# Performance work log

Measured on AMD Instinct MI355X. Metric: run time of the kernel, lower is better.

## Reference

```python
import jax, jax.numpy as jnp
import numpy as np

N_WIRES = 8
N_QLAYERS = 1
DIM = 1 << N_WIRES  # 256

# bits[s, w] = w-th bit of basis state s; wire 0 is the MOST significant bit
# (torchquantum stores states as [bsz, 2, 2, ..., 2] with wire i at axis i+1)
_BITS = ((np.arange(DIM)[:, None] >> (N_WIRES - 1 - np.arange(N_WIRES))) & 1).astype(np.float32)


def setup_inputs() -> dict:
    key = jax.random.key(0)
    ks = jax.random.split(key, 5)
    pi = float(np.pi)
    return {
        "input_features": jax.random.normal(ks[0], (4, 4096, N_WIRES), jnp.float32),
        "params_ry1": jax.random.uniform(ks[1], (N_QLAYERS, N_WIRES), jnp.float32, -pi, pi),
        "params_crz1": jax.random.uniform(ks[2], (N_QLAYERS, N_WIRES), jnp.float32, -pi, pi),
        "params_ry2": jax.random.uniform(ks[3], (N_QLAYERS, N_WIRES), jnp.float32, -pi, pi),
        "params_crz2": jax.random.uniform(ks[4], (N_QLAYERS, N_WIRES), jnp.float32, -pi, pi),
    }


def _apply_ry(state, wire, theta):
    """Apply RY(theta) = [[c,-s],[s,c]] (c=cos(theta/2)) on `wire`.
    theta: scalar (shared param) or [B] (batched encoder angle)."""
    B = state.shape[0]
    c = jnp.cos(theta * 0.5)
    s = jnp.sin(theta * 0.5)
    if jnp.ndim(theta):  # per-batch angle
        c = c[:, None, None]
        s = s[:, None, None]
    st = state.reshape(B, 1 << wire, 2, -1)
    a, b = st[:, :, 0, :], st[:, :, 1, :]
    return jnp.stack([c * a - s * b, s * a + c * b], axis=2).reshape(B, DIM)


def _crz_block_diag(controls, targets, thetas, bits):
    """Fused diagonal of a commuting block of CRZ gates.
    CRZ(c,t,th) = diag over basis: 1 if bit_c==0 else exp(+/- i th/2) for bit_t=1/0.
    exponent contribution: bit_c * th * (bit_t - 0.5)."""
    expo = (bits[:, controls] * (bits[:, targets] - 0.5)) @ thetas  # [DIM]
    return jnp.exp(1j * expo).astype(jnp.complex64)


def _vqc_forward(x, params_ry1, params_crz1, params_ry2, params_crz2):
    B = x.shape[0]
    bits = jnp.asarray(_BITS)
    # |0...0>
    state = jnp.zeros((B, DIM), jnp.complex64).at[:, 0].set(1.0)

    idx = np.arange(N_WIRES)
    ctrl1, tgt1 = idx, (idx + 1) % N_WIRES  # crz block 1: wires [i, i+1]
    ctrl2, tgt2 = idx, (idx - 1) % N_WIRES  # crz block 2: wires [i, i-1]

    for k in range(N_QLAYERS):
        # tensor-product encoder: RY(x_i) on wire i
        for i in range(N_WIRES):
            state = _apply_ry(state, i, x[:, i])
        # CRZ ring (all diagonal -> fused)
        state = state * _crz_block_diag(ctrl1, tgt1, params_crz1[k], bits)[None, :]
        # trainable RY layer 1
        for i in range(N_WIRES):
            state = _apply_ry(state, i, params_ry1[k, i])
        # reverse CRZ ring (diagonal -> fused)
        state = state * _crz_block_diag(ctrl2, tgt2, params_crz2[k], bits)[None, :]
        # trainable RY layer 2
        for i in range(N_WIRES):
            state = _apply_ry(state, i, params_ry2[k, i])

    # PauliZ expectation on every wire: <Z_w> = sum_s |amp_s|^2 * (1 - 2*bit_w(s))
    probs = (state.real ** 2 + state.imag ** 2)  # [B, DIM]
    signs = 1.0 - 2.0 * bits                      # [DIM, N_WIRES]
    return probs @ signs                          # [B, N_WIRES]


def reference(input_features, params_ry1, params_crz1, params_ry2, params_crz2):
    bsz, slen, fz = input_features.shape
    x = input_features.reshape(-1, fz)
    out = _vqc_forward(x, params_ry1, params_crz1, params_ry2, params_crz2)
    return out.reshape(bsz, slen, fz)
```

## Files before the change

kernel.cpp:

```cpp
#include <hip/hip_runtime.h>
#include <math.h>

#define NW 8

typedef float v2f __attribute__((ext_vector_type(2)));

__device__ __forceinline__ v2f mk2(float a, float b) { v2f r; r.x = a; r.y = b; return r; }

template<int CTRL>
__device__ __forceinline__ float dpp_x(float v) {
    return __int_as_float(
        __builtin_amdgcn_update_dpp(0, __float_as_int(v), CTRL, 0xF, 0xF, true));
}
template<int CTRL>
__device__ __forceinline__ v2f dpp2(v2f v) {
    v2f r;
    r.x = dpp_x<CTRL>(v.x);
    r.y = dpp_x<CTRL>(v.y);
    return r;
}
#define XCH1(v) dpp2<0xB1>(v)
#define XCH2(v) dpp2<0x4E>(v)
#define XCH8(v) dpp2<0x128>(v)

__global__ __launch_bounds__(256, 2) void vqc_kernel(
    const float* __restrict__ x,
    const float* __restrict__ ry1,
    const float* __restrict__ crz1,
    const float* __restrict__ ry2,
    const float* __restrict__ crz2,
    float* __restrict__ out,
    int B)
{
    __shared__ __align__(16) float Tc1[288], Ts1[288], Tc2[288], Ts2[288];

    const int t = threadIdx.x;
    {
        const int n = t;
        float e1 = 0.f, e2 = 0.f;
#pragma unroll
        for (int i = 0; i < NW; ++i) {
            float bc  = (float)((n >> (7 - i)) & 1);
            float bt1 = (float)((n >> (7 - ((i + 1) & 7))) & 1);
            float bt2 = (float)((n >> (7 - ((i + 7) & 7))) & 1);
            e1 += bc * crz1[i] * (bt1 - 0.5f);
            e2 += bc * crz2[i] * (bt2 - 0.5f);
        }
        const int j = n & 31;
        const int u = (((n >> 7) & 1) << 2) | (((n >> 6) & 1) << 1) | ((n >> 5) & 1);
        const int idx = u * 36 + j;
        float s, c;
        __sincosf(e1, &s, &c);  Tc1[idx] = c;  Ts1[idx] = s;
        __sincosf(e2, &s, &c);  Tc2[idx] = c;  Ts2[idx] = s;
    }
    __syncthreads();

    const int lane = t & 63;
    const int u = ((lane & 1) << 2) | (((lane >> 1) & 1) << 1) | ((lane >> 3) & 1);
    const int g = ((lane >> 3) & 6) | ((lane >> 2) & 1);

    float rc1[8], rs1[8], rc2[8], rs2[8];
#pragma unroll
    for (int i = 0; i < 8; ++i) {
        __sincosf(0.5f * ry1[i], &rs1[i], &rc1[i]);
        __sincosf(0.5f * ry2[i], &rs2[i], &rc2[i]);
    }

    const float* pc1 = &Tc1[u * 36];
    const float* ps1 = &Ts1[u * 36];
    const float* pc2 = &Tc2[u * 36];
    const float* ps2 = &Ts2[u * 36];

    const int wavesPerBlock = blockDim.x >> 6;
    const int gwave = blockIdx.x * wavesPerBlock + (t >> 6);
    const int b  = gwave * 8 + g;
    const int bl = (b < B) ? b : (B - 1);

    const float4* xp = (const float4*)(x + (size_t)bl * NW);
    float4 xa = xp[0], xb = xp[1];
    float cs[8], sn[8];
    __sincosf(0.5f * xa.x, &sn[0], &cs[0]);
    __sincosf(0.5f * xa.y, &sn[1], &cs[1]);
    __sincosf(0.5f * xa.z, &sn[2], &cs[2]);
    __sincosf(0.5f * xa.w, &sn[3], &cs[3]);
    __sincosf(0.5f * xb.x, &sn[4], &cs[4]);
    __sincosf(0.5f * xb.y, &sn[5], &cs[5]);
    __sincosf(0.5f * xb.z, &sn[6], &cs[6]);
    __sincosf(0.5f * xb.w, &sn[7], &cs[7]);

    float pcf = ((lane & 1) ? sn[0] : cs[0])
              * ((lane & 2) ? sn[1] : cs[1])
              * ((lane & 8) ? sn[2] : cs[2]);

    float t2[2], t4[4], t8[8], t16[16];
    t2[0] = pcf * cs[3];  t2[1] = pcf * sn[3];
#pragma unroll
    for (int k = 0; k < 2; ++k)  { t4[2*k]  = t2[k] * cs[4];  t4[2*k+1]  = t2[k] * sn[4]; }
#pragma unroll
    for (int k = 0; k < 4; ++k)  { t8[2*k]  = t4[k] * cs[5];  t8[2*k+1]  = t4[k] * sn[5]; }
#pragma unroll
    for (int k = 0; k < 8; ++k)  { t16[2*k] = t8[k] * cs[6];  t16[2*k+1] = t8[k] * sn[6]; }

    const v2f cw7 = mk2(cs[7], sn[7]);
    v2f aP[16];
#pragma unroll
    for (int k = 0; k < 16; ++k) aP[k] = mk2(t16[k], t16[k]) * cw7;

    v2f reP[16], imP[16];
#pragma unroll
    for (int q = 0; q < 8; ++q) {
        float4 cq = *(const float4*)&pc1[4 * q];
        float4 sq = *(const float4*)&ps1[4 * q];
        v2f cl = mk2(cq.x, cq.y), ch = mk2(cq.z, cq.w);
        v2f sl = mk2(sq.x, sq.y), sh = mk2(sq.z, sq.w);
        reP[2*q]   = aP[2*q]   * cl;  imP[2*q]   = aP[2*q]   * sl;
        reP[2*q+1] = aP[2*q+1] * ch;  imP[2*q+1] = aP[2*q+1] * sh;
    }

#define CROSS_WIRE(RC, RS, WI, LBIT, EXCH)                                  \
    { float c_ = RC[WI], s_ = RS[WI];                                       \
      float se_ = (lane & LBIT) ? s_ : -s_;                                 \
      v2f cv = mk2(c_, c_), sev = mk2(se_, se_);                            \
      _Pragma("unroll")                                                     \
      for (int k = 0; k < 16; ++k) {                                        \
          v2f pre = EXCH(reP[k]);                                           \
          v2f pim = EXCH(imP[k]);                                           \
          reP[k] = reP[k] * cv + pre * sev;                                 \
          imP[k] = imP[k] * cv + pim * sev;                                 \
      } }

#define INLANE_WIRE(RC, RS, WI, M)                                          \
    { float c_ = RC[WI], s_ = RS[WI];                                       \
      v2f cv = mk2(c_, c_), sv = mk2(s_, s_);                               \
      _Pragma("unroll")                                                     \
      for (int k = 0; k < 16; ++k) if (!(k & M)) {                          \
          int h = k | M;                                                    \
          v2f rl = reP[k], rh = reP[h], il = imP[k], ih = imP[h];           \
          reP[k] = rl * cv - rh * sv;  reP[h] = rl * sv + rh * cv;          \
          imP[k] = il * cv - ih * sv;  imP[h] = il * sv + ih * cv;          \
      } }

#define WIRE7(RC, RS)                                                       \
    { float c_ = RC[7], s_ = RS[7];                                         \
      v2f cv = mk2(c_, c_), sev = mk2(-s_, s_);                             \
      _Pragma("unroll")                                                     \
      for (int k = 0; k < 16; ++k) {                                        \
          v2f r = reP[k], i = imP[k];                                       \
          v2f rsw = mk2(r.y, r.x), isw = mk2(i.y, i.x);                     \
          reP[k] = r * cv + rsw * sev;                                      \
          imP[k] = i * cv + isw * sev;                                      \
      } }

#define RY_LAYER(RC, RS)                                                    \
    do {                                                                    \
        CROSS_WIRE(RC, RS, 0, 1, XCH1);                                     \
        CROSS_WIRE(RC, RS, 1, 2, XCH2);                                     \
        CROSS_WIRE(RC, RS, 2, 8, XCH8);                                     \
        INLANE_WIRE(RC, RS, 3, 8);                                          \
        INLANE_WIRE(RC, RS, 4, 4);                                          \
        INLANE_WIRE(RC, RS, 5, 2);                                          \
        INLANE_WIRE(RC, RS, 6, 1);                                          \
        WIRE7(RC, RS);                                                      \
    } while (0)

    RY_LAYER(rc1, rs1);

#pragma unroll
    for (int q = 0; q < 8; ++q) {
        float4 cq = *(const float4*)&pc2[4 * q];
        float4 sq = *(const float4*)&ps2[4 * q];
        v2f cl = mk2(cq.x, cq.y), ch = mk2(cq.z, cq.w);
        v2f sl = mk2(sq.x, sq.y), sh = mk2(sq.z, sq.w);
        v2f r, i;
        r = reP[2*q];   i = imP[2*q];
        reP[2*q]   = r * cl - i * sl;  imP[2*q]   = r * sl + i * cl;
        r = reP[2*q+1]; i = imP[2*q+1];
        reP[2*q+1] = r * ch - i * sh;  imP[2*q+1] = r * sh + i * ch;
    }

    RY_LAYER(rc2, rs2);

    v2f pP[16];
#pragma unroll
    for (int k = 0; k < 16; ++k) pP[k] = reP[k] * reP[k] + imP[k] * imP[k];

    v2f s1v[8], dv6 = mk2(0.f, 0.f);
#pragma unroll
    for (int k = 0; k < 8; ++k) { s1v[k] = pP[2*k] + pP[2*k+1]; dv6 += pP[2*k] - pP[2*k+1]; }
    v2f s2v[4], dv5 = mk2(0.f, 0.f);
#pragma unroll
    for (int k = 0; k < 4; ++k) { s2v[k] = s1v[2*k] + s1v[2*k+1]; dv5 += s1v[2*k] - s1v[2*k+1]; }
    v2f s3v[2], dv4 = mk2(0.f, 0.f);
#pragma unroll
    for (int k = 0; k < 2; ++k) { s3v[k] = s2v[2*k] + s2v[2*k+1]; dv4 += s2v[2*k] - s2v[2*k+1]; }
    v2f sv0 = s3v[0] + s3v[1];
    v2f dv3 = s3v[0] - s3v[1];

    float v0 = sv0.x + sv0.y, d7 = sv0.x - sv0.y;
    float d3 = dv3.x + dv3.y, d4 = dv4.x + dv4.y;
    float d5 = dv5.x + dv5.y, d6 = dv6.x + dv6.y;

    v2f w1 = mk2(v0, d3), w2 = mk2(d4, d5), w3 = mk2(d6, d7);
#define BFLY_R(EXCH, M)                                                     \
    { v2f o1 = EXCH(w1), o2 = EXCH(w2), o3 = EXCH(w3);                      \
      if (lane & M) { w1 = o1 - w1; w2 = o2 - w2; w3 = o3 - w3; }           \
      else          { w1 = o1 + w1; w2 = o2 + w2; w3 = o3 + w3; } }
    BFLY_R(XCH1, 1);
    BFLY_R(XCH2, 2);
    BFLY_R(XCH8, 8);
#undef BFLY_R

    if (b < B) {
        const int loc = lane & 11;
        float* ob = out + (size_t)b * NW;
        if      (loc == 0) { ob[3] = w1.y; *(float4*)(ob + 4) = make_float4(w2.x, w2.y, w3.x, w3.y); }
        else if (loc == 1) ob[0] = w1.x;
        else if (loc == 2) ob[1] = w1.x;
        else if (loc == 8) ob[2] = w1.x;
    }
#undef RY_LAYER
#undef CROSS_WIRE
#undef INLANE_WIRE
#undef WIRE7
}

extern "C" void kernel_launch(void* const* d_in, const int* in_sizes, int n_in,
                              void* d_out, int out_size, void* d_ws, size_t ws_size,
                              hipStream_t stream) {
    const float* x    = (const float*)d_in[0];
    const float* ry1  = (const float*)d_in[1];
    const float* crz1 = (const float*)d_in[2];
    const float* ry2  = (const float*)d_in[3];
    const float* crz2 = (const float*)d_in[4];
    float* out = (float*)d_out;

    int B = in_sizes[0] / NW;
    int blocks = (B + 31) / 32;
    if (blocks < 1) blocks = 1;
    vqc_kernel<<<blocks, 256, 0, stream>>>(x, ry1, crz1, ry2, crz2, out, B);
}
```

Baseline: 67.85 us.

## Spread each statevector over 16 lanes using permlane32 swap to halve registers

Wire 3 moves from being held inside a lane to being spread across lane halves, using a permlane32 swap (or a shuffle fallback). Each wave now simulates 4 samples instead of 8, and each lane holds 8 complex pairs instead of 16. Launch bounds rise to 4 blocks per SM, the grid doubles, and the CRZ tables are re-laid out for 16 lanes. The aim is lower register pressure and higher occupancy, at the cost of extra cross-lane exchanges and twice as many waves doing the same total work.

```diff
diff --git a/kernel.cpp b/kernel.cpp
--- a/kernel.cpp
+++ b/kernel.cpp
@@ -4,6 +4,7 @@
 #define NW 8
 
 typedef float v2f __attribute__((ext_vector_type(2)));
+typedef int   v2i __attribute__((ext_vector_type(2)));
 
 __device__ __forceinline__ v2f mk2(float a, float b) { v2f r; r.x = a; r.y = b; return r; }
 
@@ -23,7 +24,27 @@
 #define XCH2(v) dpp2<0x4E>(v)
 #define XCH8(v) dpp2<0x128>(v)
 
-__global__ __launch_bounds__(256, 2) void vqc_kernel(
+__device__ __forceinline__ float rfl(float v) {
+    return __int_as_float(__builtin_amdgcn_readfirstlane(__float_as_int(v)));
+}
+
+__device__ __forceinline__ float xch32f(float v, int lane) {
+#if __has_builtin(__builtin_amdgcn_permlane32_swap)
+    v2i r = __builtin_amdgcn_permlane32_swap(__float_as_int(v), __float_as_int(v),
+                                             false, false);
+    return __int_as_float((lane & 32) ? r[0] : r[1]);
+#else
+    return __shfl_xor(v, 32, 64);
+#endif
+}
+__device__ __forceinline__ v2f xch32_2(v2f v, int lane) {
+    v2f r;
+    r.x = xch32f(v.x, lane);
+    r.y = xch32f(v.y, lane);
+    return r;
+}
+
+__global__ __launch_bounds__(256, 4) void vqc_kernel(
     const float* __restrict__ x,
     const float* __restrict__ ry1,
     const float* __restrict__ crz1,
@@ -32,7 +53,7 @@
     float* __restrict__ out,
     int B)
 {
-    __shared__ __align__(16) float Tc1[288], Ts1[288], Tc2[288], Ts2[288];
+    __shared__ __align__(16) float Tc1[320], Ts1[320], Tc2[320], Ts2[320];
 
     const int t = threadIdx.x;
     {
@@ -46,9 +67,9 @@
             e1 += bc * crz1[i] * (bt1 - 0.5f);
             e2 += bc * crz2[i] * (bt2 - 0.5f);
         }
-        const int j = n & 31;
-        const int u = (((n >> 7) & 1) << 2) | (((n >> 6) & 1) << 1) | ((n >> 5) & 1);
-        const int idx = u * 36 + j;
+        const int j = n & 15;
+        const int u = n >> 4;
+        const int idx = u * 20 + j;
         float s, c;
         __sincosf(e1, &s, &c);  Tc1[idx] = c;  Ts1[idx] = s;
         __sincosf(e2, &s, &c);  Tc2[idx] = c;  Ts2[idx] = s;
@@ -56,24 +77,26 @@
     __syncthreads();
 
     const int lane = t & 63;
-    const int u = ((lane & 1) << 2) | (((lane >> 1) & 1) << 1) | ((lane >> 3) & 1);
-    const int g = ((lane >> 3) & 6) | ((lane >> 2) & 1);
+    const int u = ((lane & 1) << 3) | (((lane >> 1) & 1) << 2)
+                | (((lane >> 3) & 1) << 1) | ((lane >> 5) & 1);
+    const int g = ((lane >> 3) & 2) | ((lane >> 2) & 1);
 
     float rc1[8], rs1[8], rc2[8], rs2[8];
 #pragma unroll
     for (int i = 0; i < 8; ++i) {
-        __sincosf(0.5f * ry1[i], &rs1[i], &rc1[i]);
-        __sincosf(0.5f * ry2[i], &rs2[i], &rc2[i]);
-    }
-
-    const float* pc1 = &Tc1[u * 36];
-    const float* ps1 = &Ts1[u * 36];
-    const float* pc2 = &Tc2[u * 36];
-    const float* ps2 = &Ts2[u * 36];
+        float s, c;
+        __sincosf(0.5f * ry1[i], &s, &c);  rc1[i] = rfl(c);  rs1[i] = rfl(s);
+        __sincosf(0.5f * ry2[i], &s, &c);  rc2[i] = rfl(c);  rs2[i] = rfl(s);
+    }
+
+    const float* pc1 = &Tc1[u * 20];
+    const float* ps1 = &Ts1[u * 20];
+    const float* pc2 = &Tc2[u * 20];
+    const float* ps2 = &Ts2[u * 20];
 
     const int wavesPerBlock = blockDim.x >> 6;
     const int gwave = blockIdx.x * wavesPerBlock + (t >> 6);
-    const int b  = gwave * 8 + g;
+    const int b  = gwave * 4 + g;
     const int bl = (b < B) ? b : (B - 1);
 
     const float4* xp = (const float4*)(x + (size_t)bl * NW);
@@ -88,27 +111,26 @@
     __sincosf(0.5f * xb.z, &sn[6], &cs[6]);
     __sincosf(0.5f * xb.w, &sn[7], &cs[7]);
 
-    float pcf = ((lane & 1) ? sn[0] : cs[0])
-              * ((lane & 2) ? sn[1] : cs[1])
-              * ((lane & 8) ? sn[2] : cs[2]);
-
-    float t2[2], t4[4], t8[8], t16[16];
-    t2[0] = pcf * cs[3];  t2[1] = pcf * sn[3];
-#pragma unroll
-    for (int k = 0; k < 2; ++k)  { t4[2*k]  = t2[k] * cs[4];  t4[2*k+1]  = t2[k] * sn[4]; }
-#pragma unroll
-    for (int k = 0; k < 4; ++k)  { t8[2*k]  = t4[k] * cs[5];  t8[2*k+1]  = t4[k] * sn[5]; }
-#pragma unroll
-    for (int k = 0; k < 8; ++k)  { t16[2*k] = t8[k] * cs[6];  t16[2*k+1] = t8[k] * sn[6]; }
+    float pcf = ((lane & 1)  ? sn[0] : cs[0])
+              * ((lane & 2)  ? sn[1] : cs[1])
+              * ((lane & 8)  ? sn[2] : cs[2])
+              * ((lane & 32) ? sn[3] : cs[3]);
+
+    float t2[2], t4[4], t8[8];
+    t2[0] = pcf * cs[4];  t2[1] = pcf * sn[4];
+#pragma unroll
+    for (int k = 0; k < 2; ++k) { t4[2*k] = t2[k] * cs[5];  t4[2*k+1] = t2[k] * sn[5]; }
+#pragma unroll
+    for (int k = 0; k < 4; ++k) { t8[2*k] = t4[k] * cs[6];  t8[2*k+1] = t4[k] * sn[6]; }
 
     const v2f cw7 = mk2(cs[7], sn[7]);
-    v2f aP[16];
-#pragma unroll
-    for (int k = 0; k < 16; ++k) aP[k] = mk2(t16[k], t16[k]) * cw7;
-
-    v2f reP[16], imP[16];
-#pragma unroll
-    for (int q = 0; q < 8; ++q) {
+    v2f aP[8];
+#pragma unroll
+    for (int k = 0; k < 8; ++k) aP[k] = mk2(t8[k], t8[k]) * cw7;
+
+    v2f reP[8], imP[8];
+#pragma unroll
+    for (int q = 0; q < 4; ++q) {
         float4 cq = *(const float4*)&pc1[4 * q];
         float4 sq = *(const float4*)&ps1[4 * q];
         v2f cl = mk2(cq.x, cq.y), ch = mk2(cq.z, cq.w);
@@ -122,18 +144,30 @@
       float se_ = (lane & LBIT) ? s_ : -s_;                                 \
       v2f cv = mk2(c_, c_), sev = mk2(se_, se_);                            \
       _Pragma("unroll")                                                     \
-      for (int k = 0; k < 16; ++k) {                                        \
+      for (int k = 0; k < 8; ++k) {                                         \
           v2f pre = EXCH(reP[k]);                                           \
           v2f pim = EXCH(imP[k]);                                           \
           reP[k] = reP[k] * cv + pre * sev;                                 \
           imP[k] = imP[k] * cv + pim * sev;                                 \
       } }
 
+#define CROSS_WIRE32(RC, RS, WI)                                            \
+    { float c_ = RC[WI], s_ = RS[WI];                                       \
+      float se_ = (lane & 32) ? s_ : -s_;                                   \
+      v2f cv = mk2(c_, c_), sev = mk2(se_, se_);                            \
+      _Pragma("unroll")                                                     \
+      for (int k = 0; k < 8; ++k) {                                         \
+          v2f pre = xch32_2(reP[k], lane);                                  \
+          v2f pim = xch32_2(imP[k], lane);                                  \
+          reP[k] = reP[k] * cv + pre * sev;                                 \
+          imP[k] = imP[k] * cv + pim * sev;                                 \
+      } }
+
 #define INLANE_WIRE(RC, RS, WI, M)                                          \
     { float c_ = RC[WI], s_ = RS[WI];                                       \
       v2f cv = mk2(c_, c_), sv = mk2(s_, s_);                               \
       _Pragma("unroll")                                                     \
-      for (int k = 0; k < 16; ++k) if (!(k & M)) {                          \
+      for (int k = 0; k < 8; ++k) if (!(k & M)) {                           \
           int h = k | M;                                                    \
           v2f rl = reP[k], rh = reP[h], il = imP[k], ih = imP[h];           \
           reP[k] = rl * cv - rh * sv;  reP[h] = rl * sv + rh * cv;          \
@@ -144,7 +178,7 @@
     { float c_ = RC[7], s_ = RS[7];                                         \
       v2f cv = mk2(c_, c_), sev = mk2(-s_, s_);                             \
       _Pragma("unroll")                                                     \
-      for (int k = 0; k < 16; ++k) {                                        \
+      for (int k = 0; k < 8; ++k) {                                         \
           v2f r = reP[k], i = imP[k];                                       \
           v2f rsw = mk2(r.y, r.x), isw = mk2(i.y, i.x);                     \
           reP[k] = r * cv + rsw * sev;                                      \
@@ -156,7 +190,7 @@
         CROSS_WIRE(RC, RS, 0, 1, XCH1);                                     \
         CROSS_WIRE(RC, RS, 1, 2, XCH2);                                     \
         CROSS_WIRE(RC, RS, 2, 8, XCH8);                                     \
-        INLANE_WIRE(RC, RS, 3, 8);                                          \
+        CROSS_WIRE32(RC, RS, 3);                                            \
         INLANE_WIRE(RC, RS, 4, 4);                                          \
         INLANE_WIRE(RC, RS, 5, 2);                                          \
         INLANE_WIRE(RC, RS, 6, 1);                                          \
@@ -166,7 +200,7 @@
     RY_LAYER(rc1, rs1);
 
 #pragma unroll
-    for (int q = 0; q < 8; ++q) {
+    for (int q = 0; q < 4; ++q) {
         float4 cq = *(const float4*)&pc2[4 * q];
         float4 sq = *(const float4*)&ps2[4 * q];
         v2f cl = mk2(cq.x, cq.y), ch = mk2(cq.z, cq.w);
@@ -180,27 +214,24 @@
 
     RY_LAYER(rc2, rs2);
 
-    v2f pP[16];
-#pragma unroll
-    for (int k = 0; k < 16; ++k) pP[k] = reP[k] * reP[k] + imP[k] * imP[k];
-
-    v2f s1v[8], dv6 = mk2(0.f, 0.f);
-#pragma unroll
-    for (int k = 0; k < 8; ++k) { s1v[k] = pP[2*k] + pP[2*k+1]; dv6 += pP[2*k] - pP[2*k+1]; }
-    v2f s2v[4], dv5 = mk2(0.f, 0.f);
-#pragma unroll
-    for (int k = 0; k < 4; ++k) { s2v[k] = s1v[2*k] + s1v[2*k+1]; dv5 += s1v[2*k] - s1v[2*k+1]; }
-    v2f s3v[2], dv4 = mk2(0.f, 0.f);
-#pragma unroll
-    for (int k = 0; k < 2; ++k) { s3v[k] = s2v[2*k] + s2v[2*k+1]; dv4 += s2v[2*k] - s2v[2*k+1]; }
-    v2f sv0 = s3v[0] + s3v[1];
-    v2f dv3 = s3v[0] - s3v[1];
+    v2f pP[8];
+#pragma unroll
+    for (int k = 0; k < 8; ++k) pP[k] = reP[k] * reP[k] + imP[k] * imP[k];
+
+    v2f s1v[4], dv6 = mk2(0.f, 0.f);
+#pragma unroll
+    for (int k = 0; k < 4; ++k) { s1v[k] = pP[2*k] + pP[2*k+1]; dv6 += pP[2*k] - pP[2*k+1]; }
+    v2f s2v[2], dv5 = mk2(0.f, 0.f);
+#pragma unroll
+    for (int k = 0; k < 2; ++k) { s2v[k] = s1v[2*k] + s1v[2*k+1]; dv5 += s1v[2*k] - s1v[2*k+1]; }
+    v2f sv0 = s2v[0] + s2v[1];
+    v2f dv4 = s2v[0] - s2v[1];
 
     float v0 = sv0.x + sv0.y, d7 = sv0.x - sv0.y;
-    float d3 = dv3.x + dv3.y, d4 = dv4.x + dv4.y;
+    float d4 = dv4.x + dv4.y;
     float d5 = dv5.x + dv5.y, d6 = dv6.x + dv6.y;
 
-    v2f w1 = mk2(v0, d3), w2 = mk2(d4, d5), w3 = mk2(d6, d7);
+    v2f w1 = mk2(v0, d4), w2 = mk2(d5, d6), w3 = mk2(d7, 0.f);
 #define BFLY_R(EXCH, M)                                                     \
     { v2f o1 = EXCH(w1), o2 = EXCH(w2), o3 = EXCH(w3);                      \
       if (lane & M) { w1 = o1 - w1; w2 = o2 - w2; w3 = o3 - w3; }           \
@@ -208,18 +239,23 @@
     BFLY_R(XCH1, 1);
     BFLY_R(XCH2, 2);
     BFLY_R(XCH8, 8);
+    { v2f o1 = xch32_2(w1, lane), o2 = xch32_2(w2, lane), o3 = xch32_2(w3, lane);
+      if (lane & 32) { w1 = o1 - w1; w2 = o2 - w2; w3 = o3 - w3; }
+      else           { w1 = o1 + w1; w2 = o2 + w2; w3 = o3 + w3; } }
 #undef BFLY_R
 
     if (b < B) {
-        const int loc = lane & 11;
+        const int loc = lane & 43;
         float* ob = out + (size_t)b * NW;
-        if      (loc == 0) { ob[3] = w1.y; *(float4*)(ob + 4) = make_float4(w2.x, w2.y, w3.x, w3.y); }
-        else if (loc == 1) ob[0] = w1.x;
-        else if (loc == 2) ob[1] = w1.x;
-        else if (loc == 8) ob[2] = w1.x;
+        if      (loc == 0)  *(float4*)(ob + 4) = make_float4(w1.y, w2.x, w2.y, w3.x);
+        else if (loc == 1)  ob[0] = w1.x;
+        else if (loc == 2)  ob[1] = w1.x;
+        else if (loc == 8)  ob[2] = w1.x;
+        else if (loc == 32) ob[3] = w1.x;
     }
 #undef RY_LAYER
 #undef CROSS_WIRE
+#undef CROSS_WIRE32
 #undef INLANE_WIRE
 #undef WIRE7
 }
@@ -235,7 +271,7 @@
     float* out = (float*)d_out;
 
     int B = in_sizes[0] / NW;
-    int blocks = (B + 31) / 32;
+    int blocks = (B + 15) / 16;
     if (blocks < 1) blocks = 1;
     vqc_kernel<<<blocks, 256, 0, stream>>>(x, ry1, crz1, ry2, crz2, out, B);
 }
```

After: 72.19 us. 6.4% more time.
